# Optimization experiments

Hardware: AMD Instinct MI355X
Metric: run time of the kernel (lower is better)

## Reference

```python
import jax, jax.numpy as jnp
import numpy as np

_INV_SQRT_2PI = 1.0 / np.sqrt(2.0 * np.pi)


def dtriple(w, noise, scale):
    # stochastic ternary: triple(w - scale*noise) = (q>1) - (q<-1)
    q = w - scale * noise
    return (q > 1).astype(jnp.float32) - (q < -1).astype(jnp.float32)


def setup_inputs() -> dict:
    key = jax.random.key(0)
    ks = jax.random.split(key, 5)
    B, D_IN, D_H, D_OUT = 4096, 1024, 16384, 3 * 32 * 32
    return {
        "x": jax.random.normal(ks[0], (B, D_IN), dtype=jnp.float32),
        "w1": jax.random.normal(ks[1], (D_IN, D_H), dtype=jnp.float32),
        "s1": jnp.ones((D_H,), dtype=jnp.float32) / 32.0,
        "b1": jnp.zeros((D_H,), dtype=jnp.float32),
        "w2": jax.random.normal(ks[2], (D_H, D_OUT), dtype=jnp.float32),
        "s2": jnp.ones((D_OUT,), dtype=jnp.float32) / np.sqrt(D_OUT).astype(np.float32),
        "b2": jnp.zeros((D_OUT,), dtype=jnp.float32),
        "n1": jax.random.normal(ks[3], (D_IN, D_H), dtype=jnp.float32),
        "n2": jax.random.normal(ks[4], (D_H, D_OUT), dtype=jnp.float32),
        "scale": 1,
    }


def reference(x, w1, s1, b1, w2, s2, b2, n1, n2, scale):
    scale = jnp.float32(scale)
    weight1 = s1 * dtriple(w1, n1, scale)          # [1024, 16384]
    h = jnp.tanh(x @ weight1 + b1)                 # [B, 16384]
    weight2 = s2 * dtriple(w2, n2, scale)          # [16384, 3072]
    out = h @ weight2 + b2                         # [B, 3072]
    return out.reshape((-1, 3, 32, 32))
```

## Files before the change

### kernel.cpp

```cpp
#include <hip/hip_runtime.h>


typedef __bf16 bf16x8 __attribute__((ext_vector_type(8)));
typedef float f32x16 __attribute__((ext_vector_type(16)));

#define AS1 __attribute__((address_space(1)))
#define AS3 __attribute__((address_space(3)))

__device__ __forceinline__ void gload_lds16(const void* g, void* l) {
    __builtin_amdgcn_global_load_lds((AS1 const void*)g, (AS3 void*)l, 16, 0, 0);
}

__device__ __forceinline__ unsigned short f2bf(float f) {
    union { float f; unsigned int u; } v; v.f = f;
    unsigned int u = v.u;
    unsigned int r = u + 0x7fffu + ((u >> 16) & 1u);
    return (unsigned short)(r >> 16);
}

__device__ __forceinline__ unsigned short tern_bf(float q) {
    return (q > 1.f) ? 0x3F80u : ((q < -1.f) ? 0xBF80u : 0u);
}

__device__ __forceinline__ float load_scale(const void* p) {
    int i = *(const int*)p;
    if (i >= -1000000 && i <= 1000000) return (float)i;
    union { int i; float f; } v; v.i = i; return v.f;
}

__device__ __forceinline__ float tanh_fast(float x) {
    float e = __expf(2.0f * x);
    return 1.0f - 2.0f * __builtin_amdgcn_rcpf(e + 1.0f);
}

__global__ __launch_bounds__(256) void pack_x_kernel(
    const float* __restrict__ x, unsigned short* __restrict__ out)
{
    const int kt = blockIdx.x, mt = blockIdx.y, tid = threadIdx.x;
    unsigned short* chunk = out + (size_t)(mt * 32 + kt) * 4096;
#pragma unroll
    for (int it = 0; it < 2; it++) {
        int g = tid + it * 256;
        int s = g >> 7, r = g & 127, h = (r >> 6) & 1, ln = r & 63;
        int m = s * 32 + (ln & 31), k = h * 16 + (ln >> 5) * 8;
        const float* src = x + (size_t)(mt * 128 + m) * 1024 + kt * 32 + k;
        float4 v0 = *(const float4*)src;
        float4 v1 = *(const float4*)(src + 4);
        unsigned int w0 = (unsigned int)f2bf(v0.x) | ((unsigned int)f2bf(v0.y) << 16);
        unsigned int w1 = (unsigned int)f2bf(v0.z) | ((unsigned int)f2bf(v0.w) << 16);
        unsigned int w2 = (unsigned int)f2bf(v1.x) | ((unsigned int)f2bf(v1.y) << 16);
        unsigned int w3 = (unsigned int)f2bf(v1.z) | ((unsigned int)f2bf(v1.w) << 16);
        uint4 o; o.x = w0; o.y = w1; o.z = w2; o.w = w3;
        *(uint4*)&chunk[(size_t)g * 8] = o;
    }
}

__global__ __launch_bounds__(256) void quant_pack_w(
    const float* __restrict__ w, const float* __restrict__ nz,
    const void* __restrict__ scale_ptr,
    unsigned short* __restrict__ out, int N, int Kt)
{
    __shared__ unsigned short lt[128 * 34];
    const int kt = blockIdx.x, nt = blockIdx.y, tid = threadIdx.x;
    const float scale = load_scale(scale_ptr);
#pragma unroll
    for (int it = 0; it < 4; it++) {
        int p = it * 1024 + tid * 4;
        int kr = p >> 7, nc = p & 127;
        size_t g = (size_t)(kt * 32 + kr) * N + nt * 128 + nc;
        float4 wv = *(const float4*)(w + g);
        float4 nv = *(const float4*)(nz + g);
        lt[(nc + 0) * 34 + kr] = tern_bf(wv.x - scale * nv.x);
        lt[(nc + 1) * 34 + kr] = tern_bf(wv.y - scale * nv.y);
        lt[(nc + 2) * 34 + kr] = tern_bf(wv.z - scale * nv.z);
        lt[(nc + 3) * 34 + kr] = tern_bf(wv.w - scale * nv.w);
    }
    __syncthreads();
    unsigned short* chunk = out + (size_t)(nt * Kt + kt) * 4096;
#pragma unroll
    for (int it = 0; it < 2; it++) {
        int g = tid + it * 256;
        int s = g >> 7, r = g & 127, h = (r >> 6) & 1, ln = r & 63;
        int n = s * 32 + (ln & 31), k = h * 16 + (ln >> 5) * 8;
        const unsigned int* p32 = (const unsigned int*)&lt[n * 34 + k];
        uint4 o; o.x = p32[0]; o.y = p32[1]; o.z = p32[2]; o.w = p32[3];
        *(uint4*)&chunk[(size_t)g * 8] = o;
    }
}


#define VMCNT(n) asm volatile("s_waitcnt vmcnt(" #n ")" ::: "memory")
#define BARRIER() { asm volatile("" ::: "memory"); __builtin_amdgcn_s_barrier(); asm volatile("" ::: "memory"); }

#define RD_FRAG(dst, HALF, SUB, P)                                            \
    dst[0] = *(const bf16x8*)&lds[P][HALF][(SUB)*1024 + lane*8];              \
    dst[1] = *(const bf16x8*)&lds[P][HALF][(SUB)*1024 + 512 + lane*8];        \
    dst[2] = *(const bf16x8*)&lds[P][HALF][4096 + (SUB)*1024 + lane*8];       \
    dst[3] = *(const bf16x8*)&lds[P][HALF][4096 + (SUB)*1024 + 512 + lane*8];

#define MFMA4(ci, cj, av, bv)                                                 \
    acc[ci][cj] = __builtin_amdgcn_mfma_f32_32x32x16_bf16(av[0], bv[0], acc[ci][cj], 0,0,0); \
    acc[ci][cj] = __builtin_amdgcn_mfma_f32_32x32x16_bf16(av[1], bv[1], acc[ci][cj], 0,0,0); \
    acc[ci][cj] = __builtin_amdgcn_mfma_f32_32x32x16_bf16(av[2], bv[2], acc[ci][cj], 0,0,0); \
    acc[ci][cj] = __builtin_amdgcn_mfma_f32_32x32x16_bf16(av[3], bv[3], acc[ci][cj], 0,0,0);

#define GSTEP(P, Q, T, WA, WB, WC, DO_STAGE)                                  \
  {                                                   \
    if (DO_STAGE) STAGE(Q, 0, (T) + 1);                                       \
    WA; BARRIER();                                                            \
    RD_FRAG(fa0, 0, sA, P); RD_FRAG(fa1, 0, sA + 1, P);                       \
    RD_FRAG(fb0, 2, sB, P); RD_FRAG(fb1, 3, sB, P);                           \
    __builtin_amdgcn_s_setprio(1);                                            \
    MFMA4(0, 0, fa0, fb0); MFMA4(1, 0, fa1, fb0);                             \
    __builtin_amdgcn_s_setprio(0);                                            \
    if (DO_STAGE) STAGE(Q, 2, (T) + 1);                                       \
    WB;                                                                       \
    __builtin_amdgcn_s_setprio(1);                                            \
    MFMA4(0, 1, fa0, fb1); MFMA4(1, 1, fa1, fb1);                             \
    __builtin_amdgcn_s_setprio(0);                                            \
                                                      \
    if (DO_STAGE) STAGE(Q, 3, (T) + 1);                                       \
    BARRIER();                                                                \
    RD_FRAG(fa0, 1, sA, P); RD_FRAG(fa1, 1, sA + 1, P);                       \
    __builtin_amdgcn_s_setprio(1);                                            \
    MFMA4(2, 1, fa0, fb1); MFMA4(3, 1, fa1, fb1);                             \
    __builtin_amdgcn_s_setprio(0);                                            \
    if (DO_STAGE) STAGE(Q, 1, (T) + 1);                                       \
    WC;                                                                       \
    __builtin_amdgcn_s_setprio(1);                                            \
    MFMA4(2, 0, fa0, fb0); MFMA4(3, 0, fa1, fb0);                             \
    __builtin_amdgcn_s_setprio(0);                                            \
  }

#define NOWAIT ((void)0)

__global__ __launch_bounds__(512, 2) void gemm1_256_kernel(
    const unsigned short* __restrict__ Ap,
    const unsigned short* __restrict__ Bp,
    unsigned short* __restrict__ Hq,
    const float* __restrict__ s1v, const float* __restrict__ b1v)
{
    __shared__ unsigned short lds[2][4][8192];
    const int tid = threadIdx.x;
    const int lane = tid & 63, wave = tid >> 6;
    const int bid0 = blockIdx.x + 16 * blockIdx.y;
    const int wg = (bid0 & 7) * 128 + (bid0 >> 3);
    const int NT = wg & 15;
    const int MT = wg >> 4;
    const int wm = ((wave >> 2) & 1) * 64;
    const int sA = wm >> 5;
    const int sB = wave & 3;

    f32x16 acc[4][2] = {};

    const unsigned short* Ab = Ap + ((size_t)(2 * MT) * 32) * 4096;
    const unsigned short* Bb = Bp + ((size_t)(2 * NT) * 32) * 4096;

    auto STAGE = [&](int q, int half, int t) {
        const unsigned short* g = (half < 2)
            ? (Ab + ((size_t)(half * 32 + 2 * t)) * 4096)
            : (Bb + ((size_t)((half - 2) * 32 + 2 * t)) * 4096);
        unsigned short* l = &lds[q][half][0];
        gload_lds16(g + tid * 8,        l + tid * 8);
        gload_lds16(g + 4096 + tid * 8, l + 4096 + tid * 8);
    };

    bf16x8 fa0[4], fa1[4], fb0[4], fb1[4];

    STAGE(0, 0, 0); STAGE(0, 2, 0); STAGE(0, 3, 0); STAGE(0, 1, 0);

    for (int t = 0; t < 14; t += 2) {
        GSTEP(0, 1, t,     VMCNT(4), VMCNT(4), VMCNT(4), true);
        GSTEP(1, 0, t + 1, VMCNT(4), VMCNT(4), VMCNT(4), true);
    }
    GSTEP(0, 1, 14, VMCNT(4), VMCNT(4), VMCNT(4), true);
    GSTEP(1, 0, 15, VMCNT(2), VMCNT(0), NOWAIT,  false);

    __syncthreads();

    const int mloc = lane & 31, hi = lane >> 5;
    unsigned int* stg32 = (unsigned int*)&lds[0][0][0];
#pragma unroll
    for (int i = 0; i < 4; i++) {
        const int kc  = (i >> 1) * 4 + sA + (i & 1);
        const int k2b = MT * 256 + (i >> 1) * 128 + wm + (i & 1) * 32;
#pragma unroll
        for (int j = 0; j < 2; j++) {
#pragma unroll
            for (int c = 0; c < 8; c++) {
                const int n1off = 8 * (c >> 1) + 4 * hi + 2 * (c & 1);
                const int n1g = k2b + n1off;
                float t0 = tanh_fast(s1v[n1g]     * acc[i][j][2 * c]     + b1v[n1g]);
                float t1 = tanh_fast(s1v[n1g + 1] * acc[i][j][2 * c + 1] + b1v[n1g + 1]);
                unsigned int pw = (unsigned int)f2bf(t0)
                                | ((unsigned int)f2bf(t1) << 16);
                const int a32 = (j * 8 + kc) * 2048 + sB * 512
                              + ((c >> 2) & 1) * 256 + ((c >> 1) & 1) * 128
                              + mloc * 4 + 2 * hi + (c & 1);
                stg32[a32] = pw;
            }
        }
    }
    __syncthreads();

#pragma unroll
    for (int mg = 0; mg < 2; mg++) {
        uint4* dst = (uint4*)(Hq + ((size_t)(2 * NT + mg) * 512 + MT * 8) * 4096);
        const uint4* src = (const uint4*)&lds[0][0][0];
#pragma unroll
        for (int it = 0; it < 8; it++)
            dst[it * 512 + tid] = src[mg * 4096 + it * 512 + tid];
    }
}

__global__ __launch_bounds__(512, 2) void gemm2_256_kernel(
    const unsigned short* __restrict__ Ap,
    const unsigned short* __restrict__ Bp,
    float* __restrict__ out,
    const float* __restrict__ s2, const float* __restrict__ b2,
    int nstep)
{
    __shared__ unsigned short lds[2][4][8192];
    const int tid = threadIdx.x;
    const int lane = tid & 63, wave = tid >> 6;
    const int bid0 = blockIdx.x + 12 * blockIdx.y;
    const int wg = (bid0 & 7) * 24 + (bid0 >> 3);
    const int NT = wg % 12;
    const int MT = wg / 12;
    const int wm = ((wave >> 2) & 1) * 64;
    const int sA = wm >> 5;
    const int sB = wave & 3;

    f32x16 acc[4][2] = {};

    const unsigned short* Ab = Ap + ((size_t)(2 * MT) * 512) * 4096;
    const unsigned short* Bb = Bp + ((size_t)(2 * NT) * 512) * 4096;

    auto STAGE = [&](int q, int half, int t) {
        const unsigned short* g = (half < 2)
            ? (Ab + ((size_t)(half * 512 + 2 * t)) * 4096)
            : (Bb + ((size_t)((half - 2) * 512 + 2 * t)) * 4096);
        unsigned short* l = &lds[q][half][0];
        gload_lds16(g + tid * 8,        l + tid * 8);
        gload_lds16(g + 4096 + tid * 8, l + 4096 + tid * 8);
    };

    bf16x8 fa0[4], fa1[4], fb0[4], fb1[4];

    STAGE(0, 0, 0); STAGE(0, 2, 0); STAGE(0, 3, 0); STAGE(0, 1, 0);

    for (int t = 0; t < nstep - 2; t += 2) {
        GSTEP(0, 1, t,     VMCNT(4), VMCNT(4), VMCNT(4), true);
        GSTEP(1, 0, t + 1, VMCNT(4), VMCNT(4), VMCNT(4), true);
    }
    GSTEP(0, 1, nstep - 2, VMCNT(4), VMCNT(4), VMCNT(4), true);
    GSTEP(1, 0, nstep - 1, VMCNT(2), VMCNT(0), NOWAIT,  false);

    const int l31 = lane & 31;
    const int rowb = 4 * (lane >> 5);
#pragma unroll
    for (int j = 0; j < 2; j++) {
        int n = NT * 256 + j * 128 + sB * 32 + l31;
        float sc = s2[n], bb = b2[n];
#pragma unroll
        for (int i = 0; i < 4; i++) {
            int mbase = MT * 256 + (i >> 1) * 128 + wm + (i & 1) * 32;
#pragma unroll
            for (int reg = 0; reg < 16; reg++) {
                int m = mbase + (reg & 3) + 8 * (reg >> 2) + rowb;
                out[(size_t)m * 3072 + n] = sc * acc[i][j][reg] + bb;
            }
        }
    }
}

extern "C" void kernel_launch(void* const* d_in, const int* in_sizes, int n_in,
                              void* d_out, int out_size, void* d_ws, size_t ws_size,
                              hipStream_t stream) {
    const float* x  = (const float*)d_in[0];
    const float* w1 = (const float*)d_in[1];
    const float* s1 = (const float*)d_in[2];
    const float* b1 = (const float*)d_in[3];
    const float* w2 = (const float*)d_in[4];
    const float* s2 = (const float*)d_in[5];
    const float* b2 = (const float*)d_in[6];
    const float* n1 = (const float*)d_in[7];
    const float* n2 = (const float*)d_in[8];
    const void* scale_p = d_in[9];
    float* out = (float*)d_out;

    if (ws_size < (264ull << 20)) return;
    unsigned char* ws = (unsigned char*)d_ws;
    unsigned short* xq  = (unsigned short*)(ws);
    unsigned short* w1q = (unsigned short*)(ws + (8ull << 20));
    unsigned short* hq  = (unsigned short*)(ws + (40ull << 20));
    unsigned short* w2q = (unsigned short*)(ws + (168ull << 20));

    pack_x_kernel<<<dim3(32, 32), 256, 0, stream>>>(x, xq);
    quant_pack_w<<<dim3(32, 128), 256, 0, stream>>>(w1, n1, scale_p, w1q, 16384, 32);
    quant_pack_w<<<dim3(512, 24), 256, 0, stream>>>(w2, n2, scale_p, w2q, 3072, 512);

    gemm1_256_kernel<<<dim3(16, 64), 512, 0, stream>>>(w1q, xq, hq, s1, b1);
    gemm2_256_kernel<<<dim3(12, 16), 512, 0, stream>>>(hq, w2q, out, s2, b2, 256);
}
```

Before: 1.028 ms.

## Retile second GEMM to 256x192 tiles to fill all compute units

Replaces the 256x256-tile second GEMM (192 workgroups) with a 256x192-tile version launched as 256 workgroups, so every compute unit gets one tile. The wave layout changes to a 4x2 grid, each wave computing 2x3 MFMA 32x32 blocks, with new staging of B sub-panels and a reworked pipelined step schedule and wait counts. The smaller tile lowers per-tile data reuse and changes LDS layout and register use.

```diff
diff --git a/kernel.cpp b/kernel.cpp
--- a/kernel.cpp
+++ b/kernel.cpp
@@ -88,9 +88,9 @@
     }
 }
 
-
 #define VMCNT(n) asm volatile("s_waitcnt vmcnt(" #n ")" ::: "memory")
 #define BARRIER() { asm volatile("" ::: "memory"); __builtin_amdgcn_s_barrier(); asm volatile("" ::: "memory"); }
+#define NOWAIT ((void)0)
 
 #define RD_FRAG(dst, HALF, SUB, P)                                            \
     dst[0] = *(const bf16x8*)&lds[P][HALF][(SUB)*1024 + lane*8];              \
@@ -132,8 +132,6 @@
     __builtin_amdgcn_s_setprio(0);                                            \
   }
 
-#define NOWAIT ((void)0)
-
 __global__ __launch_bounds__(512, 2) void gemm1_256_kernel(
     const unsigned short* __restrict__ Ap,
     const unsigned short* __restrict__ Bp,
@@ -213,58 +211,109 @@
     }
 }
 
-__global__ __launch_bounds__(512, 2) void gemm2_256_kernel(
+__global__ __launch_bounds__(512, 2) void gemm2_192_kernel(
     const unsigned short* __restrict__ Ap,
     const unsigned short* __restrict__ Bp,
     float* __restrict__ out,
-    const float* __restrict__ s2, const float* __restrict__ b2,
-    int nstep)
+    const float* __restrict__ s2, const float* __restrict__ b2)
 {
-    __shared__ unsigned short lds[2][4][8192];
+    __shared__ unsigned short lds[2][28672];
     const int tid = threadIdx.x;
     const int lane = tid & 63, wave = tid >> 6;
-    const int bid0 = blockIdx.x + 12 * blockIdx.y;
-    const int wg = (bid0 & 7) * 24 + (bid0 >> 3);
-    const int NT = wg % 12;
-    const int MT = wg / 12;
-    const int wm = ((wave >> 2) & 1) * 64;
-    const int sA = wm >> 5;
-    const int sB = wave & 3;
-
-    f32x16 acc[4][2] = {};
-
-    const unsigned short* Ab = Ap + ((size_t)(2 * MT) * 512) * 4096;
-    const unsigned short* Bb = Bp + ((size_t)(2 * NT) * 512) * 4096;
-
-    auto STAGE = [&](int q, int half, int t) {
-        const unsigned short* g = (half < 2)
-            ? (Ab + ((size_t)(half * 512 + 2 * t)) * 4096)
-            : (Bb + ((size_t)((half - 2) * 512 + 2 * t)) * 4096);
-        unsigned short* l = &lds[q][half][0];
-        gload_lds16(g + tid * 8,        l + tid * 8);
-        gload_lds16(g + 4096 + tid * 8, l + 4096 + tid * 8);
+    const int bid0 = blockIdx.x + 16 * blockIdx.y;
+    const int wg = (bid0 & 7) * 32 + (bid0 >> 3);
+    const int NT = wg & 15;
+    const int MT = wg >> 4;
+    const int wM = wave >> 1;
+    const int wN = wave & 1;
+
+    f32x16 acc[2][3] = {};
+
+    const unsigned short* Abase = Ap + ((size_t)(2 * MT) * 512) * 4096;
+
+    auto STAGE_A = [&](int q, int r, int kc, int t) {
+        const unsigned short* g = Abase + ((size_t)(r * 512 + 2 * t + kc)) * 4096;
+        unsigned short* l = &lds[q][kc * 8192 + r * 4096];
+        gload_lds16(g + tid * 8, l + tid * 8);
     };
-
-    bf16x8 fa0[4], fa1[4], fb0[4], fb1[4];
-
-    STAGE(0, 0, 0); STAGE(0, 2, 0); STAGE(0, 3, 0); STAGE(0, 1, 0);
-
-    for (int t = 0; t < nstep - 2; t += 2) {
-        GSTEP(0, 1, t,     VMCNT(4), VMCNT(4), VMCNT(4), true);
-        GSTEP(1, 0, t + 1, VMCNT(4), VMCNT(4), VMCNT(4), true);
-    }
-    GSTEP(0, 1, nstep - 2, VMCNT(4), VMCNT(4), VMCNT(4), true);
-    GSTEP(1, 0, nstep - 1, VMCNT(2), VMCNT(0), NOWAIT,  false);
+    auto STAGE_B = [&](int q, int p, int t) {
+        int f = p * 512 + tid;
+        int u6 = f >> 8, within = f & 255;
+        int kc = (u6 >= 3) ? 1 : 0;
+        int u3 = u6 - 3 * kc;
+        int u_abs = 3 * NT + u3;
+        const unsigned short* g = Bp
+            + ((size_t)((u_abs >> 1) * 512 + 2 * t + kc)) * 4096
+            + (u_abs & 1) * 2048 + within * 8;
+        unsigned short* l = &lds[q][16384 + f * 8];
+        gload_lds16(g, l);
+    };
+
+    bf16x8 fa[2][2], fb[3][2];
+#define RDA(i, kc, P) {                                                        \
+    int sub = 2 * wM + (i);                                                    \
+    const unsigned short* a = &lds[P][(kc) * 8192 + (sub >> 2) * 4096          \
+                                      + (sub & 3) * 1024 + lane * 8];          \
+    fa[i][0] = *(const bf16x8*)a; fa[i][1] = *(const bf16x8*)(a + 512); }
+#define RDB(j, kc, P) {                                                        \
+    int s = 3 * wN + (j);                                                      \
+    const unsigned short* b = &lds[P][16384 + (kc) * 6144 + (s >> 1) * 2048    \
+                                      + (s & 1) * 1024 + lane * 8];            \
+    fb[j][0] = *(const bf16x8*)b; fb[j][1] = *(const bf16x8*)(b + 512); }
+#define MFMA2G(ci, cj)                                                         \
+    acc[ci][cj] = __builtin_amdgcn_mfma_f32_32x32x16_bf16(fa[ci][0], fb[cj][0], acc[ci][cj], 0,0,0); \
+    acc[ci][cj] = __builtin_amdgcn_mfma_f32_32x32x16_bf16(fa[ci][1], fb[cj][1], acc[ci][cj], 0,0,0);
+
+#define GS192(P, Q, T, W1, W2, W3, DO_STAGE)                                   \
+  {                                          \
+    if (DO_STAGE) { STAGE_A(Q, 0, 0, (T) + 1); STAGE_A(Q, 1, 0, (T) + 1); }    \
+    W1; BARRIER();                                                             \
+    RDA(0, 0, P); RDA(1, 0, P);                                                \
+    RDB(0, 0, P); RDB(1, 0, P); RDB(2, 0, P);                                  \
+    __builtin_amdgcn_s_setprio(1);                                             \
+    MFMA2G(0, 0); MFMA2G(0, 1); MFMA2G(0, 2);                                  \
+    __builtin_amdgcn_s_setprio(0);                                             \
+    if (DO_STAGE) { STAGE_B(Q, 0, (T) + 1); STAGE_B(Q, 1, (T) + 1); }          \
+    W2;                                                                        \
+    __builtin_amdgcn_s_setprio(1);                                             \
+    MFMA2G(1, 0); MFMA2G(1, 1); MFMA2G(1, 2);                                  \
+    __builtin_amdgcn_s_setprio(0);                                             \
+                                             \
+    if (DO_STAGE) { STAGE_A(Q, 0, 1, (T) + 1); STAGE_A(Q, 1, 1, (T) + 1); }    \
+    BARRIER();                                                                 \
+    RDA(0, 1, P); RDA(1, 1, P);                                                \
+    RDB(0, 1, P); RDB(1, 1, P); RDB(2, 1, P);                                  \
+    __builtin_amdgcn_s_setprio(1);                                             \
+    MFMA2G(0, 0); MFMA2G(0, 1); MFMA2G(0, 2);                                  \
+    __builtin_amdgcn_s_setprio(0);                                             \
+    if (DO_STAGE) STAGE_B(Q, 2, (T) + 1);                                      \
+    W3;                                                                        \
+    __builtin_amdgcn_s_setprio(1);                                             \
+    MFMA2G(1, 0); MFMA2G(1, 1); MFMA2G(1, 2);                                  \
+    __builtin_amdgcn_s_setprio(0);                                             \
+  }
+
+    STAGE_A(0, 0, 0, 0); STAGE_A(0, 1, 0, 0);
+    STAGE_B(0, 0, 0);    STAGE_B(0, 1, 0);
+    STAGE_A(0, 0, 1, 0); STAGE_A(0, 1, 1, 0);
+    STAGE_B(0, 2, 0);
+
+    for (int t = 0; t < 254; t += 2) {
+        GS192(0, 1, t,     VMCNT(3), VMCNT(4), VMCNT(3), true);
+        GS192(1, 0, t + 1, VMCNT(3), VMCNT(4), VMCNT(3), true);
+    }
+    GS192(0, 1, 254, VMCNT(3), VMCNT(4), VMCNT(3), true);
+    GS192(1, 0, 255, VMCNT(0), NOWAIT,   NOWAIT,  false);
 
     const int l31 = lane & 31;
     const int rowb = 4 * (lane >> 5);
 #pragma unroll
-    for (int j = 0; j < 2; j++) {
-        int n = NT * 256 + j * 128 + sB * 32 + l31;
+    for (int j = 0; j < 3; j++) {
+        int n = NT * 192 + wN * 96 + j * 32 + l31;
         float sc = s2[n], bb = b2[n];
 #pragma unroll
-        for (int i = 0; i < 4; i++) {
-            int mbase = MT * 256 + (i >> 1) * 128 + wm + (i & 1) * 32;
+        for (int i = 0; i < 2; i++) {
+            int mbase = MT * 256 + wM * 64 + i * 32;
 #pragma unroll
             for (int reg = 0; reg < 16; reg++) {
                 int m = mbase + (reg & 3) + 8 * (reg >> 2) + rowb;
@@ -272,6 +321,10 @@
             }
         }
     }
+#undef RDA
+#undef RDB
+#undef MFMA2G
+#undef GS192
 }
 
 extern "C" void kernel_launch(void* const* d_in, const int* in_sizes, int n_in,
@@ -301,5 +354,5 @@
     quant_pack_w<<<dim3(512, 24), 256, 0, stream>>>(w2, n2, scale_p, w2q, 3072, 512);
 
     gemm1_256_kernel<<<dim3(16, 64), 512, 0, stream>>>(w1q, xq, hq, s1, b1);
-    gemm2_256_kernel<<<dim3(12, 16), 512, 0, stream>>>(hq, w2q, out, s2, b2, 256);
-}
+    gemm2_192_kernel<<<dim3(16, 16), 512, 0, stream>>>(hq, w2q, out, s2, b2);
+}
```

Result: faster. 997.1 us (-3.0%).

## Quantize hidden activations to int8 and run second GEMM with i8 MFMA

Applied to the files above, without the earlier changes.

The first GEMM epilogue now stores tanh outputs as int8 scaled by 127 instead of bf16. A new packing kernel emits the ternary second-layer weights as int8. The second GEMM is rewritten to use 32x32x32 i8 MFMA with a 256x192 tile and rescales by s2/127 in the epilogue. This halves the hidden-activation traffic and uses the higher int8 matrix throughput, at the cost of quantization error in the hidden activations.

```diff
diff --git a/kernel.cpp b/kernel.cpp
--- a/kernel.cpp
+++ b/kernel.cpp
@@ -3,6 +3,8 @@
 
 typedef __bf16 bf16x8 __attribute__((ext_vector_type(8)));
 typedef float f32x16 __attribute__((ext_vector_type(16)));
+typedef int i32x4 __attribute__((ext_vector_type(4)));
+typedef int i32x16 __attribute__((ext_vector_type(16)));
 
 #define AS1 __attribute__((address_space(1)))
 #define AS3 __attribute__((address_space(3)))
@@ -61,7 +63,7 @@
     unsigned short* __restrict__ out, int N, int Kt)
 {
     __shared__ unsigned short lt[128 * 34];
-    const int kt = blockIdx.x, nt = blockIdx.y, tid = threadIdx.x;
+    const int nt = blockIdx.x, kt = blockIdx.y, tid = threadIdx.x;
     const float scale = load_scale(scale_ptr);
 #pragma unroll
     for (int it = 0; it < 4; it++) {
@@ -88,9 +90,49 @@
     }
 }
 
+__global__ __launch_bounds__(256) void quant_pack_w2_i8(
+    const float* __restrict__ w, const float* __restrict__ nz,
+    const void* __restrict__ scale_ptr, unsigned char* __restrict__ out)
+{
+    const int nt = blockIdx.x, ktp = blockIdx.y, tid = threadIdx.x;
+    const int c = tid >> 7, r = tid & 127, ng = r & 31, kg = r >> 5;
+    const int kt = ktp * 2 + c;
+    const float scale = load_scale(scale_ptr);
+    const int k0 = kt * 32 + kg * 8;
+    const int n0 = nt * 128 + ng * 4;
+
+    int us[8][4];
+#pragma unroll
+    for (int i = 0; i < 8; i++) {
+        size_t g = (size_t)(k0 + i) * 3072 + n0;
+        float4 wv = *(const float4*)(w + g);
+        float4 nv = *(const float4*)(nz + g);
+        float q0 = wv.x - scale * nv.x, q1 = wv.y - scale * nv.y;
+        float q2 = wv.z - scale * nv.z, q3 = wv.w - scale * nv.w;
+        us[i][0] = (q0 > 1.f) - (q0 < -1.f);
+        us[i][1] = (q1 > 1.f) - (q1 < -1.f);
+        us[i][2] = (q2 > 1.f) - (q2 < -1.f);
+        us[i][3] = (q3 > 1.f) - (q3 < -1.f);
+    }
+
+    unsigned char* chunk = out + (size_t)(nt * 512 + kt) * 4096;
+    const int hi = kg >> 1, eb = (kg & 1) * 8;
+#pragma unroll
+    for (int j = 0; j < 4; j++) {
+        int nl = ng * 4 + j;
+        int addr = (nl >> 5) * 1024 + (hi * 32 + (nl & 31)) * 16 + eb;
+        unsigned int lo = (us[0][j] & 255) | ((us[1][j] & 255) << 8)
+                        | ((us[2][j] & 255) << 16) | ((us[3][j] & 255) << 24);
+        unsigned int hw = (us[4][j] & 255) | ((us[5][j] & 255) << 8)
+                        | ((us[6][j] & 255) << 16) | ((us[7][j] & 255) << 24);
+        uint2 o; o.x = lo; o.y = hw;
+        *(uint2*)&chunk[addr] = o;
+    }
+}
 
 #define VMCNT(n) asm volatile("s_waitcnt vmcnt(" #n ")" ::: "memory")
 #define BARRIER() { asm volatile("" ::: "memory"); __builtin_amdgcn_s_barrier(); asm volatile("" ::: "memory"); }
+#define NOWAIT ((void)0)
 
 #define RD_FRAG(dst, HALF, SUB, P)                                            \
     dst[0] = *(const bf16x8*)&lds[P][HALF][(SUB)*1024 + lane*8];              \
@@ -105,8 +147,7 @@
     acc[ci][cj] = __builtin_amdgcn_mfma_f32_32x32x16_bf16(av[3], bv[3], acc[ci][cj], 0,0,0);
 
 #define GSTEP(P, Q, T, WA, WB, WC, DO_STAGE)                                  \
-  {                                                   \
-    if (DO_STAGE) STAGE(Q, 0, (T) + 1);                                       \
+  { if (DO_STAGE) STAGE(Q, 0, (T) + 1);                                       \
     WA; BARRIER();                                                            \
     RD_FRAG(fa0, 0, sA, P); RD_FRAG(fa1, 0, sA + 1, P);                       \
     RD_FRAG(fb0, 2, sB, P); RD_FRAG(fb1, 3, sB, P);                           \
@@ -118,7 +159,6 @@
     __builtin_amdgcn_s_setprio(1);                                            \
     MFMA4(0, 1, fa0, fb1); MFMA4(1, 1, fa1, fb1);                             \
     __builtin_amdgcn_s_setprio(0);                                            \
-                                                      \
     if (DO_STAGE) STAGE(Q, 3, (T) + 1);                                       \
     BARRIER();                                                                \
     RD_FRAG(fa0, 1, sA, P); RD_FRAG(fa1, 1, sA + 1, P);                       \
@@ -132,12 +172,10 @@
     __builtin_amdgcn_s_setprio(0);                                            \
   }
 
-#define NOWAIT ((void)0)
-
 __global__ __launch_bounds__(512, 2) void gemm1_256_kernel(
     const unsigned short* __restrict__ Ap,
     const unsigned short* __restrict__ Bp,
-    unsigned short* __restrict__ Hq,
+    unsigned char* __restrict__ Hq,
     const float* __restrict__ s1v, const float* __restrict__ b1v)
 {
     __shared__ unsigned short lds[2][4][8192];
@@ -187,17 +225,18 @@
 #pragma unroll
         for (int j = 0; j < 2; j++) {
 #pragma unroll
-            for (int c = 0; c < 8; c++) {
-                const int n1off = 8 * (c >> 1) + 4 * hi + 2 * (c & 1);
-                const int n1g = k2b + n1off;
-                float t0 = tanh_fast(s1v[n1g]     * acc[i][j][2 * c]     + b1v[n1g]);
-                float t1 = tanh_fast(s1v[n1g + 1] * acc[i][j][2 * c + 1] + b1v[n1g + 1]);
-                unsigned int pw = (unsigned int)f2bf(t0)
-                                | ((unsigned int)f2bf(t1) << 16);
-                const int a32 = (j * 8 + kc) * 2048 + sB * 512
-                              + ((c >> 2) & 1) * 256 + ((c >> 1) & 1) * 128
-                              + mloc * 4 + 2 * hi + (c & 1);
-                stg32[a32] = pw;
+            for (int g = 0; g < 4; g++) {
+                unsigned int pw = 0;
+#pragma unroll
+                for (int rr = 0; rr < 4; rr++) {
+                    const int n1g = k2b + rr + 8 * g + 4 * hi;
+                    float t = tanh_fast(s1v[n1g] * acc[i][j][4 * g + rr] + b1v[n1g]);
+                    int q = __float2int_rn(t * 127.0f);
+                    pw |= ((unsigned int)(q & 255)) << (8 * rr);
+                }
+                const int w32 = (j * 8 + kc) * 1024 + sB * 256 + (g >> 1) * 128
+                              + mloc * 4 + (g & 1) * 2 + hi;
+                stg32[w32] = pw;
             }
         }
     }
@@ -205,73 +244,122 @@
 
 #pragma unroll
     for (int mg = 0; mg < 2; mg++) {
-        uint4* dst = (uint4*)(Hq + ((size_t)(2 * NT + mg) * 512 + MT * 8) * 4096);
+        uint4* dst = (uint4*)(Hq + ((size_t)((2 * NT + mg) * 512 + MT * 8)) * 4096);
         const uint4* src = (const uint4*)&lds[0][0][0];
 #pragma unroll
-        for (int it = 0; it < 8; it++)
-            dst[it * 512 + tid] = src[mg * 4096 + it * 512 + tid];
-    }
-}
-
-__global__ __launch_bounds__(512, 2) void gemm2_256_kernel(
-    const unsigned short* __restrict__ Ap,
-    const unsigned short* __restrict__ Bp,
+        for (int it = 0; it < 4; it++)
+            dst[it * 512 + tid] = src[mg * 2048 + it * 512 + tid];
+    }
+}
+
+__global__ __launch_bounds__(512, 2) void gemm2_192_i8(
+    const unsigned char* __restrict__ Ap,
+    const unsigned char* __restrict__ Bp,
     float* __restrict__ out,
-    const float* __restrict__ s2, const float* __restrict__ b2,
-    int nstep)
-{
-    __shared__ unsigned short lds[2][4][8192];
+    const float* __restrict__ s2, const float* __restrict__ b2)
+{
+    __shared__ unsigned char lds[2][28672];
     const int tid = threadIdx.x;
     const int lane = tid & 63, wave = tid >> 6;
-    const int bid0 = blockIdx.x + 12 * blockIdx.y;
-    const int wg = (bid0 & 7) * 24 + (bid0 >> 3);
-    const int NT = wg % 12;
-    const int MT = wg / 12;
-    const int wm = ((wave >> 2) & 1) * 64;
-    const int sA = wm >> 5;
-    const int sB = wave & 3;
-
-    f32x16 acc[4][2] = {};
-
-    const unsigned short* Ab = Ap + ((size_t)(2 * MT) * 512) * 4096;
-    const unsigned short* Bb = Bp + ((size_t)(2 * NT) * 512) * 4096;
-
-    auto STAGE = [&](int q, int half, int t) {
-        const unsigned short* g = (half < 2)
-            ? (Ab + ((size_t)(half * 512 + 2 * t)) * 4096)
-            : (Bb + ((size_t)((half - 2) * 512 + 2 * t)) * 4096);
-        unsigned short* l = &lds[q][half][0];
-        gload_lds16(g + tid * 8,        l + tid * 8);
-        gload_lds16(g + 4096 + tid * 8, l + 4096 + tid * 8);
-    };
-
-    bf16x8 fa0[4], fa1[4], fb0[4], fb1[4];
-
-    STAGE(0, 0, 0); STAGE(0, 2, 0); STAGE(0, 3, 0); STAGE(0, 1, 0);
-
-    for (int t = 0; t < nstep - 2; t += 2) {
-        GSTEP(0, 1, t,     VMCNT(4), VMCNT(4), VMCNT(4), true);
-        GSTEP(1, 0, t + 1, VMCNT(4), VMCNT(4), VMCNT(4), true);
-    }
-    GSTEP(0, 1, nstep - 2, VMCNT(4), VMCNT(4), VMCNT(4), true);
-    GSTEP(1, 0, nstep - 1, VMCNT(2), VMCNT(0), NOWAIT,  false);
+    const int bid0 = blockIdx.x + 16 * blockIdx.y;
+    const int wg = (bid0 & 7) * 32 + (bid0 >> 3);
+    const int NT = wg & 15;
+    const int MT = wg >> 4;
+    const int wM = wave >> 1, wN = wave & 1;
+
+    i32x16 acc[2][3] = {};
+
+    const unsigned char* Abase = Ap + ((size_t)(2 * MT) * 512) * 4096;
+    const int ar = tid >> 8, aw = (tid & 255) * 16;
+
+    auto boff = [&](int f) -> size_t {
+        int kc = (f >= 384);
+        int rem = f * 16 - kc * 6144;
+        int u = rem >> 11, wi = rem & 2047;
+        int uab = 3 * NT + u;
+        return ((size_t)((uab >> 1) * 512 + kc)) * 4096 + (uab & 1) * 2048 + wi;
+    };
+    const size_t b0o = boff(tid);
+    const size_t b1o = boff(512 + (tid & 255));
+    const int b0d = 16384 + tid * 16;
+    const int b1d = 16384 + (512 + (tid & 255)) * 16;
+
+    auto STAGE_A = [&](int q, int kc, int t) {
+        gload_lds16(Abase + ((size_t)(ar * 512 + kc)) * 4096 + aw + (size_t)t * 8192,
+                    &lds[q][kc * 8192 + ar * 4096 + aw]);
+    };
+    auto STAGE_B0 = [&](int q, int t) {
+        gload_lds16(Bp + b0o + (size_t)t * 8192, &lds[q][b0d]);
+    };
+    auto STAGE_B1 = [&](int q, int t) {
+        gload_lds16(Bp + b1o + (size_t)t * 8192, &lds[q][b1d]);
+    };
+
+    i32x4 fa[2], fb[3];
+#define RDA8(i, kc, P) {                                                       \
+    int sub = 2 * wM + (i);                                                    \
+    fa[i] = *(const i32x4*)&lds[P][(kc) * 8192 + (sub >> 2) * 4096             \
+                                   + (sub & 3) * 1024 + lane * 16]; }
+#define RDB8(j, kc, P)                                                         \
+    fb[j] = *(const i32x4*)&lds[P][16384 + (kc) * 6144 + (3 * wN + (j)) * 1024 \
+                                   + lane * 16];
+#define MFMA8(ci, cj)                                                          \
+    acc[ci][cj] = __builtin_amdgcn_mfma_i32_32x32x32_i8(fa[ci], fb[cj], acc[ci][cj], 0, 0, 0);
+
+#define GS8(P, Q, T, W1, W3, DO_STAGE)                                         \
+  { if (DO_STAGE) STAGE_A(Q, 0, (T) + 1);                                      \
+    W1; BARRIER();                                                             \
+    RDA8(0, 0, P); RDA8(1, 0, P);                                              \
+    RDB8(0, 0, P); RDB8(1, 0, P); RDB8(2, 0, P);                               \
+    __builtin_amdgcn_s_setprio(1);                                             \
+    MFMA8(0, 0); MFMA8(0, 1); MFMA8(0, 2);                                     \
+    __builtin_amdgcn_s_setprio(0);                                             \
+    if (DO_STAGE) STAGE_B0(Q, (T) + 1);                                        \
+    __builtin_amdgcn_s_setprio(1);                                             \
+    MFMA8(1, 0); MFMA8(1, 1); MFMA8(1, 2);                                     \
+    __builtin_amdgcn_s_setprio(0);                                             \
+    if (DO_STAGE) STAGE_A(Q, 1, (T) + 1);                                      \
+    W3; BARRIER();                                                             \
+    RDA8(0, 1, P); RDA8(1, 1, P);                                              \
+    RDB8(0, 1, P); RDB8(1, 1, P); RDB8(2, 1, P);                               \
+    __builtin_amdgcn_s_setprio(1);                                             \
+    MFMA8(0, 0); MFMA8(0, 1); MFMA8(0, 2);                                     \
+    __builtin_amdgcn_s_setprio(0);                                             \
+    if (DO_STAGE) STAGE_B1(Q, (T) + 1);                                        \
+    __builtin_amdgcn_s_setprio(1);                                             \
+    MFMA8(1, 0); MFMA8(1, 1); MFMA8(1, 2);                                     \
+    __builtin_amdgcn_s_setprio(0);                                             \
+  }
+
+    STAGE_A(0, 0, 0); STAGE_B0(0, 0); STAGE_A(0, 1, 0); STAGE_B1(0, 0);
+
+    for (int t = 0; t < 254; t += 2) {
+        GS8(0, 1, t,     VMCNT(3), VMCNT(3), true);
+        GS8(1, 0, t + 1, VMCNT(3), VMCNT(3), true);
+    }
+    GS8(0, 1, 254, VMCNT(3), VMCNT(3), true);
+    GS8(1, 0, 255, VMCNT(2), VMCNT(0), false);
 
     const int l31 = lane & 31;
     const int rowb = 4 * (lane >> 5);
 #pragma unroll
-    for (int j = 0; j < 2; j++) {
-        int n = NT * 256 + j * 128 + sB * 32 + l31;
-        float sc = s2[n], bb = b2[n];
-#pragma unroll
-        for (int i = 0; i < 4; i++) {
-            int mbase = MT * 256 + (i >> 1) * 128 + wm + (i & 1) * 32;
+    for (int j = 0; j < 3; j++) {
+        int n = NT * 192 + wN * 96 + j * 32 + l31;
+        float sc = s2[n] * (1.0f / 127.0f), bb = b2[n];
+#pragma unroll
+        for (int i = 0; i < 2; i++) {
+            int mbase = MT * 256 + wM * 64 + i * 32;
 #pragma unroll
             for (int reg = 0; reg < 16; reg++) {
                 int m = mbase + (reg & 3) + 8 * (reg >> 2) + rowb;
-                out[(size_t)m * 3072 + n] = sc * acc[i][j][reg] + bb;
+                out[(size_t)m * 3072 + n] = sc * (float)acc[i][j][reg] + bb;
             }
         }
     }
+#undef RDA8
+#undef RDB8
+#undef MFMA8
+#undef GS8
 }
 
 extern "C" void kernel_launch(void* const* d_in, const int* in_sizes, int n_in,
@@ -293,13 +381,13 @@
     unsigned char* ws = (unsigned char*)d_ws;
     unsigned short* xq  = (unsigned short*)(ws);
     unsigned short* w1q = (unsigned short*)(ws + (8ull << 20));
-    unsigned short* hq  = (unsigned short*)(ws + (40ull << 20));
-    unsigned short* w2q = (unsigned short*)(ws + (168ull << 20));
+    unsigned char*  hq  = (unsigned char*)(ws + (40ull << 20));
+    unsigned char*  w2q = (unsigned char*)(ws + (104ull << 20));
 
     pack_x_kernel<<<dim3(32, 32), 256, 0, stream>>>(x, xq);
-    quant_pack_w<<<dim3(32, 128), 256, 0, stream>>>(w1, n1, scale_p, w1q, 16384, 32);
-    quant_pack_w<<<dim3(512, 24), 256, 0, stream>>>(w2, n2, scale_p, w2q, 3072, 512);
+    quant_pack_w<<<dim3(128, 32), 256, 0, stream>>>(w1, n1, scale_p, w1q, 16384, 32);
+    quant_pack_w2_i8<<<dim3(24, 256), 256, 0, stream>>>(w2, n2, scale_p, w2q);
 
     gemm1_256_kernel<<<dim3(16, 64), 512, 0, stream>>>(w1q, xq, hq, s1, b1);
-    gemm2_256_kernel<<<dim3(12, 16), 512, 0, stream>>>(hq, w2q, out, s2, b2, 256);
-}
+    gemm2_192_i8<<<dim3(16, 16), 512, 0, stream>>>(hq, w2q, out, s2, b2);
+}
```

Measured after the change: 831.6 us. 19.1% less time.
